# Optimization experiments

Measured on AMD Instinct MI355X. Metric: run time of the kernel, lower is better.

The kernel has to match this reference:

```python
import jax, jax.numpy as jnp
import numpy as np

B, T, D = 2, 2048, 2048
H, DH, DR, DL = 16, 128, 64, 512
WINDOW, STRIDE, GLOBAL = 512, 64, 128
BASE, MAX_SEQ, ORIG_MAX = 10000.0, 131072, 4096
BETA_FAST, BETA_SLOW = 32.0, 1.0
SCALE = 1.0 / np.sqrt(DH)
SCALE_ROPE = 1.0 / np.sqrt(DR)


def _yarn_inv_freq():
    base_inv = 1.0 / (BASE ** (np.arange(0, DR, 2, dtype=np.float32) / DR))
    scale = MAX_SEQ / ORIG_MAX
    freqs = np.arange(DR // 2, dtype=np.float32)
    ramp = np.clip((freqs - BETA_SLOW) / (BETA_FAST - BETA_SLOW), 0.0, 1.0)
    return jnp.asarray(base_inv * (1 - ramp) + (base_inv / scale) * ramp)

_INV_FREQ = _yarn_inv_freq()
_YARN_FACTOR = np.float32(0.1 * np.log(MAX_SEQ / ORIG_MAX) + 1.0)


def _apply_rope(x):
    # x: [B, H, T, DR]
    t = jnp.arange(x.shape[2], dtype=jnp.float32)
    fr = t[:, None] * _INV_FREQ[None, :]            # [T, DR/2]
    emb = jnp.concatenate([fr, fr], axis=-1)        # [T, DR]
    cos, sin = jnp.cos(emb), jnp.sin(emb)
    x1, x2 = jnp.split(x, 2, axis=-1)
    rot = jnp.concatenate([-x2, x1], axis=-1)
    return (x * cos + rot * sin) * _YARN_FACTOR


def _sparse_mask(seq_len):
    pos = jnp.arange(seq_len)
    qp, kp = pos[:, None], pos[None, :]
    dist = qp - kp
    half = WINDOW // 2
    window = (dist >= -half) & (dist <= half)
    dilated = (kp % STRIDE == 0) | (kp < GLOBAL)
    causal = kp <= qp
    return (window | dilated) & causal              # [T, T] bool


def setup_inputs() -> dict:
    key = jax.random.key(0)
    ks = jax.random.split(key, 9)
    s = 0.02
    return {
        "x": jax.random.normal(ks[0], (B, T, D), jnp.float32),
        "w_q": jax.random.normal(ks[1], (D, D), jnp.float32) * s,
        "w_dkv": jax.random.normal(ks[2], (D, DL), jnp.float32) * s,
        "w_uk": jax.random.normal(ks[3], (DL, D), jnp.float32) * s,
        "w_uv": jax.random.normal(ks[4], (DL, D), jnp.float32) * s,
        "w_q_pos": jax.random.normal(ks[5], (D, H * DR), jnp.float32) * s,
        "w_k_pos": jax.random.normal(ks[6], (D, H * DR), jnp.float32) * s,
        "w_o": jax.random.normal(ks[7], (D, D), jnp.float32) * s,
    }


def reference(x, w_q, w_dkv, w_uk, w_uv, w_q_pos, w_k_pos, w_o):
    b, t, _ = x.shape
    # MLA projections
    q_c = (x @ w_q).reshape(b, t, H, DH).transpose(0, 2, 1, 3)      # [B,H,T,DH]
    c_kv = x @ w_dkv                                                # [B,T,DL]
    k_c = (c_kv @ w_uk).reshape(b, t, H, DH).transpose(0, 2, 1, 3)
    v_c = (c_kv @ w_uv).reshape(b, t, H, DH).transpose(0, 2, 1, 3)
    # decoupled RoPE branch (YaRN)
    q_r = (x @ w_q_pos).reshape(b, t, H, DR).transpose(0, 2, 1, 3)
    k_r = (x @ w_k_pos).reshape(b, t, H, DR).transpose(0, 2, 1, 3)
    q_r = _apply_rope(q_r)
    k_r = _apply_rope(k_r)
    # combined content + positional scores
    scores = jnp.einsum("bhqd,bhkd->bhqk", q_c, k_c) * SCALE \
           + jnp.einsum("bhqr,bhkr->bhqk", q_r, k_r) * SCALE_ROPE
    mask = _sparse_mask(t)                                          # [T,T]
    scores = jnp.where(mask[None, None], scores, -jnp.inf)
    attn = jax.nn.softmax(scores, axis=-1)
    out = jnp.einsum("bhqk,bhkd->bhqd", attn, v_c)                  # [B,H,T,DH]
    out = out.transpose(0, 2, 1, 3).reshape(b, t, D)
    return out @ w_o
```

## Files before the change

### kernel.cpp

```cpp
#include <hip/hip_runtime.h>
#include <hip/hip_bf16.h>
#include <cstdint>

typedef __attribute__((ext_vector_type(8))) short short8_t;
typedef __attribute__((ext_vector_type(4))) short short4_t;
typedef __attribute__((ext_vector_type(4))) float f32x4_t;

#define AS1 __attribute__((address_space(1)))
#define AS3 __attribute__((address_space(3)))

__device__ __forceinline__ void gload_lds16(const void* g, void* l) {
  __builtin_amdgcn_global_load_lds((const AS1 void*)g, (AS3 void*)l, 16, 0, 0);
}

__device__ __forceinline__ short8_t ld8(const __hip_bfloat16* p) {
  return *(const short8_t*)p;
}

__global__ __launch_bounds__(256) void k_prep(
    const float* __restrict__ x, __hip_bfloat16* __restrict__ xb,
    const float* __restrict__ wq,  const float* __restrict__ wqp,
    const float* __restrict__ wkp, const float* __restrict__ wdkv,
    const float* __restrict__ wuk, const float* __restrict__ wuv,
    const float* __restrict__ wo,
    __hip_bfloat16* __restrict__ Bt1, __hip_bfloat16* __restrict__ Bt2,
    __hip_bfloat16* __restrict__ woT) {
  __shared__ float t[64][65];
  int bid = blockIdx.x;
  if (bid < 4096) {
    int i = (bid * 256 + threadIdx.x) * 8;
    union { short8_t v; __hip_bfloat16 h[8]; } u;
#pragma unroll
    for (int j = 0; j < 8; ++j) u.h[j] = __float2bfloat16(x[i + j]);
    *(short8_t*)(xb + i) = u.v;
    return;
  }
  bid -= 4096;
  const float* in; __hip_bfloat16* out; int R, C, tile;
  if (bid < 1024)      { in = wq;   out = Bt1;                 R = 2048; C = 2048; tile = bid; }
  else if (bid < 1536) { in = wqp;  out = Bt1 + 2048UL * 2048; R = 2048; C = 1024; tile = bid - 1024; }
  else if (bid < 2048) { in = wkp;  out = Bt1 + 3072UL * 2048; R = 2048; C = 1024; tile = bid - 1536; }
  else if (bid < 2304) { in = wdkv; out = Bt1 + 4096UL * 2048; R = 2048; C = 512;  tile = bid - 2048; }
  else if (bid < 2560) { in = wuk;  out = Bt2;                 R = 512;  C = 2048; tile = bid - 2304; }
  else if (bid < 2816) { in = wuv;  out = Bt2 + 2048UL * 512;  R = 512;  C = 2048; tile = bid - 2560; }
  else                 { in = wo;   out = woT;                 R = 2048; C = 2048; tile = bid - 2816; }
  int nct = C >> 6;
  int ct = tile % nct, rt = tile / nct;
  int r0 = rt << 6, c0 = ct << 6;
#pragma unroll
  for (int i = 0; i < 16; ++i) {
    int idx = i * 256 + threadIdx.x;
    int r = idx >> 6, c = idx & 63;
    t[r][c] = in[(size_t)(r0 + r) * C + c0 + c];
  }
  __syncthreads();
#pragma unroll
  for (int i = 0; i < 16; ++i) {
    int idx = i * 256 + threadIdx.x;
    int c = idx >> 6, r = idx & 63;
    out[(size_t)(c0 + c) * R + r0 + r] = __float2bfloat16(t[r][c]);
  }
}

template<int MODE>
__global__ __launch_bounds__(256) void k_gemm2(const __hip_bfloat16* __restrict__ A,
                                               const __hip_bfloat16* __restrict__ Bt,
                                               int K, int nbx,
                                               void* __restrict__ O0, void* __restrict__ O1,
                                               void* __restrict__ O2, void* __restrict__ O3,
                                               float alpha) {
  __shared__ __align__(16) __hip_bfloat16 Al[3][128 * 32];
  __shared__ __align__(16) __hip_bfloat16 Bl[3][128 * 32];
  int bx = blockIdx.x % nbx, by = blockIdx.x / nbx;
  int tid = threadIdx.x, lane = tid & 63, w = tid >> 6;
  int L = lane & 15, hi = lane >> 4;
  int wr = (w >> 1) << 6, wc = (w & 1) << 6;
  f32x4_t acc[4][4] = {};
  const __hip_bfloat16* Ag = A + (size_t)(by * 128) * K;
  const __hip_bfloat16* Bg = Bt + (size_t)(bx * 128) * K;
  int rA = w * 16 + (lane >> 2);
  int cA = ((lane & 3) ^ ((lane >> 3) & 3)) * 8;
  int NT = K >> 5;

  auto stage = [&](int s) {
    int j = s % 3;
    int k0 = s << 5;
    gload_lds16(Ag + (size_t)rA * K + k0 + cA,        &Al[j][(w * 16) * 32]);
    gload_lds16(Ag + (size_t)(rA + 64) * K + k0 + cA, &Al[j][(64 + w * 16) * 32]);
    gload_lds16(Bg + (size_t)rA * K + k0 + cA,        &Bl[j][(w * 16) * 32]);
    gload_lds16(Bg + (size_t)(rA + 64) * K + k0 + cA, &Bl[j][(64 + w * 16) * 32]);
  };

  stage(0); stage(1);
  asm volatile("s_waitcnt vmcnt(4)\ns_barrier" ::: "memory");

  int hs = hi ^ ((L >> 1) & 3);
  for (int t = 0; t < NT; ++t) {
    int j = t % 3;
    short8_t af[4], bf[4];
#pragma unroll
    for (int m = 0; m < 4; ++m) af[m] = ld8(&Al[j][(wr + 16 * m + L) * 32 + 8 * hs]);
#pragma unroll
    for (int n = 0; n < 4; ++n) bf[n] = ld8(&Bl[j][(wc + 16 * n + L) * 32 + 8 * hs]);
    if (t + 2 < NT) stage(t + 2);
    __builtin_amdgcn_s_setprio(1);
#pragma unroll
    for (int m = 0; m < 4; ++m)
#pragma unroll
      for (int n = 0; n < 4; ++n)
        acc[m][n] = __builtin_amdgcn_mfma_f32_16x16x32_bf16(af[m], bf[n], acc[m][n], 0, 0, 0);
    __builtin_amdgcn_s_setprio(0);
    if (t + 2 < NT)      asm volatile("s_waitcnt vmcnt(4)\ns_barrier" ::: "memory");
    else if (t + 1 < NT) asm volatile("s_waitcnt vmcnt(0)\ns_barrier" ::: "memory");
  }

  int r0 = by * 128 + wr + 4 * hi;
  int cb = bx * 128 + wc;

  if (MODE == 1) {
    float* C = (float*)O0;
    size_t N = (size_t)nbx << 7;
#pragma unroll
    for (int m = 0; m < 4; ++m)
#pragma unroll
      for (int n = 0; n < 4; ++n)
#pragma unroll
        for (int i = 0; i < 4; ++i)
          C[(size_t)(r0 + 16 * m + i) * N + cb + 16 * n + L] = acc[m][n][i] * alpha;
  } else if (MODE == 2) {
    __hip_bfloat16* qcb = (__hip_bfloat16*)O0;
    __hip_bfloat16* qrb = (__hip_bfloat16*)O1;
    __hip_bfloat16* krb = (__hip_bfloat16*)O2;
    __hip_bfloat16* ckv = (__hip_bfloat16*)O3;
    if (bx < 16) {
      const float SCALE = 0.08838834764831845f;
#pragma unroll
      for (int m = 0; m < 4; ++m)
#pragma unroll
        for (int n = 0; n < 4; ++n)
#pragma unroll
          for (int i = 0; i < 4; ++i)
            qcb[(size_t)(r0 + 16 * m + i) * 2048 + cb + 16 * n + L] =
                __float2bfloat16(acc[m][n][i] * SCALE);
    } else if (bx < 32) {
      bool isq = bx < 24;
      __hip_bfloat16* dst = isq ? qrb : krb;
      float osc = isq ? 0.16832169878499666f : 1.3465735902799727f;
      int cbl = cb - (isq ? 2048 : 3072);
      float invf[2];
#pragma unroll
      for (int p = 0; p < 2; ++p) {
        float fi = (float)(16 * p + L);
        float bi = __expf(fi * -0.28782313662425574f);
        float ramp = fminf(fmaxf((fi - 1.0f) * (1.0f / 31.0f), 0.0f), 1.0f);
        invf[p] = bi * (1.0f - ramp * (31.0f / 32.0f));
      }
#pragma unroll
      for (int m = 0; m < 4; ++m)
#pragma unroll
        for (int i = 0; i < 4; ++i) {
          int row = r0 + 16 * m + i;
          float ft = (float)(row & 2047);
#pragma unroll
          for (int p = 0; p < 2; ++p) {
            float sn, cs;
            __sincosf(ft * invf[p], &sn, &cs);
            float x1 = acc[m][p][i], x2 = acc[m][p + 2][i];
            dst[(size_t)row * 1024 + cbl + 16 * p + L] =
                __float2bfloat16((x1 * cs - x2 * sn) * osc);
            dst[(size_t)row * 1024 + cbl + 32 + 16 * p + L] =
                __float2bfloat16((x2 * cs + x1 * sn) * osc);
          }
        }
    } else {
      int cbl = cb - 4096;
#pragma unroll
      for (int m = 0; m < 4; ++m)
#pragma unroll
        for (int n = 0; n < 4; ++n)
#pragma unroll
          for (int i = 0; i < 4; ++i)
            ckv[(size_t)(r0 + 16 * m + i) * 512 + cbl + 16 * n + L] =
                __float2bfloat16(acc[m][n][i]);
    }
  } else if (MODE == 3) {
    __hip_bfloat16* kcb = (__hip_bfloat16*)O0;
    __hip_bfloat16* vcb = (__hip_bfloat16*)O1;
    __hip_bfloat16* vT  = (__hip_bfloat16*)O2;
    if (bx < 16) {
#pragma unroll
      for (int m = 0; m < 4; ++m)
#pragma unroll
        for (int n = 0; n < 4; ++n)
#pragma unroll
          for (int i = 0; i < 4; ++i)
            kcb[(size_t)(r0 + 16 * m + i) * 2048 + cb + 16 * n + L] =
                __float2bfloat16(acc[m][n][i]);
    } else {
#pragma unroll
      for (int m = 0; m < 4; ++m)
#pragma unroll
        for (int n = 0; n < 4; ++n) {
          int vcol = cb - 2048 + 16 * n + L;
          int hh = vcol >> 7, dh = vcol & 127;
          int row0 = r0 + 16 * m;
          int b = row0 >> 11, t0 = row0 & 2047;
          union { short4_t v; __hip_bfloat16 h4[4]; } pk;
#pragma unroll
          for (int i = 0; i < 4; ++i) {
            __hip_bfloat16 bv = __float2bfloat16(acc[m][n][i]);
            vcb[(size_t)(row0 + i) * 2048 + vcol] = bv;
            pk.h4[i] = bv;
          }
          *(short4_t*)(vT + ((size_t)((b * 16 + hh) * 128 + dh) * 2048 + t0)) = pk.v;
        }
    }
  }
}

__global__ __launch_bounds__(256) void k_attn(const __hip_bfloat16* __restrict__ qc,
                                              const __hip_bfloat16* __restrict__ kc,
                                              const __hip_bfloat16* __restrict__ vcb,
                                              const __hip_bfloat16* __restrict__ qr,
                                              const __hip_bfloat16* __restrict__ kr,
                                              const __hip_bfloat16* __restrict__ vT,
                                              __hip_bfloat16* __restrict__ ao) {
  const int T = 2048;
  int bid = blockIdx.x;
  int xcd = bid & 7, r = bid >> 3;
  int j = r >> 5, qt = r & 31;
  int bh = xcd + 8 * j;
  int b = bh >> 4, h = bh & 15;
  int tid = threadIdx.x, lane = tid & 63, w = tid >> 6;
  int L = lane & 15, hi = lane >> 4;
  int q0 = qt * 64;

  __shared__ __align__(16) __hip_bfloat16 Kl[64 * 200];
  __shared__ __align__(16) __hip_bfloat16 Vt[128 * 64];
  __shared__ __align__(16) __hip_bfloat16 Pl[4][16 * 72];

  char* Vtb = (char*)Vt;
  const __hip_bfloat16* vTb = vT + (size_t)(b * 16 + h) * 128 * 2048;

  int qrow = q0 + w * 16 + L;
  size_t qb = (size_t)b * T + qrow;
  short8_t qf[6];
#pragma unroll
  for (int c = 0; c < 4; ++c)
    qf[c] = ld8(qc + qb * 2048 + h * 128 + 32 * c + 8 * hi);
#pragma unroll
  for (int c = 0; c < 2; ++c)
    qf[4 + c] = ld8(qr + qb * 1024 + h * 64 + 32 * c + 8 * hi);

  f32x4_t oacc[8] = {};
  float mrow[4], lrow[4];
#pragma unroll
  for (int i = 0; i < 4; ++i) { mrow[i] = -1e30f; lrow[i] = 0.0f; }

  int nd = qt - 6;

  for (int step = 0; step <= qt + 1; ++step) {
    bool compact = (step == qt + 1);
    if (compact && nd <= 0) break;
    int kt = step;
    if (!compact && kt > 1 && kt < qt - 4) continue;
    int k0 = kt * 64;

    if (!compact) {
#pragma unroll
      for (int i = 0; i < 6; ++i) {
        int ch = i * 256 + tid;
        int rr = ch / 24;
        int d = (ch % 24) * 8;
        size_t krow = (size_t)b * T + k0 + rr;
        const __hip_bfloat16* src = (d < 128)
            ? kc + krow * 2048 + h * 128 + d
            : kr + krow * 1024 + h * 64 + (d - 128);
        *(short8_t*)(Kl + rr * 200 + d) = ld8(src);
      }
#pragma unroll
      for (int i = 0; i < 4; ++i) {
        int ch = i * 256 + tid;
        int row = ch >> 3, c = ch & 7;
        int swc = c ^ (row & 7);
        *(short8_t*)(Vtb + row * 128 + 16 * swc) = ld8(vTb + (size_t)row * 2048 + k0 + c * 8);
      }
    } else {
#pragma unroll
      for (int i = 0; i < 6; ++i) {
        int ch = i * 256 + tid;
        int rr = ch / 24;
        int d = (ch % 24) * 8;
        int srcr = (rr < nd) ? 64 * (2 + rr) : 0;
        size_t krow = (size_t)b * T + srcr;
        const __hip_bfloat16* src = (d < 128)
            ? kc + krow * 2048 + h * 128 + d
            : kr + krow * 1024 + h * 64 + (d - 128);
        *(short8_t*)(Kl + rr * 200 + d) = ld8(src);
      }
#pragma unroll
      for (int i = 0; i < 2; ++i) {
        int ch = i * 256 + tid;
        int jj = ch >> 4, d0 = (ch & 15) * 8;
        if (jj < nd) {
          union { short8_t v; __hip_bfloat16 hh[8]; } u;
          u.v = ld8(vcb + (size_t)(b * 2048 + 64 * (2 + jj)) * 2048 + h * 128 + d0);
#pragma unroll
          for (int qq = 0; qq < 8; ++qq) {
            int dh = d0 + qq;
            int swc = (jj >> 3) ^ (dh & 7);
            *(__hip_bfloat16*)(Vtb + dh * 128 + 16 * swc + 2 * (jj & 7)) = u.hh[qq];
          }
        }
      }
    }
    __syncthreads();

    f32x4_t sacc[4] = {};
    __builtin_amdgcn_s_setprio(1);
#pragma unroll
    for (int n = 0; n < 4; ++n)
#pragma unroll
      for (int c = 0; c < 6; ++c) {
        short8_t bfr = ld8(Kl + (16 * n + L) * 200 + 32 * c + 8 * hi);
        sacc[n] = __builtin_amdgcn_mfma_f32_16x16x32_bf16(qf[c], bfr, sacc[n], 0, 0, 0);
      }
    __builtin_amdgcn_s_setprio(0);

    int rbase = q0 + w * 16 + 4 * hi;
    float p[4][4];
    float mt[4];
#pragma unroll
    for (int i = 0; i < 4; ++i) mt[i] = -1e30f;
#pragma unroll
    for (int n = 0; n < 4; ++n) {
      int col = L + 16 * n;
      int k = k0 + col;
#pragma unroll
      for (int i = 0; i < 4; ++i) {
        int rq = rbase + i;
        bool ok = compact ? (col < nd)
                          : ((k <= rq) && ((rq - k <= 256) || ((k & 63) == 0) || (k < 128)));
        float s = ok ? sacc[n][i] : -1e30f;
        p[n][i] = s;
        mt[i] = fmaxf(mt[i], s);
      }
    }
    for (int d = 1; d < 16; d <<= 1)
#pragma unroll
      for (int i = 0; i < 4; ++i) mt[i] = fmaxf(mt[i], __shfl_xor(mt[i], d, 64));
    float al[4], rs[4];
#pragma unroll
    for (int i = 0; i < 4; ++i) {
      float mnew = fmaxf(mrow[i], mt[i]);
      al[i] = __expf(mrow[i] - mnew);
      mrow[i] = mnew;
      rs[i] = 0.0f;
    }
#pragma unroll
    for (int n = 0; n < 4; ++n)
#pragma unroll
      for (int i = 0; i < 4; ++i) {
        float e = __expf(p[n][i] - mrow[i]);
        p[n][i] = e;
        rs[i] += e;
      }
    for (int d = 1; d < 16; d <<= 1)
#pragma unroll
      for (int i = 0; i < 4; ++i) rs[i] += __shfl_xor(rs[i], d, 64);
#pragma unroll
    for (int i = 0; i < 4; ++i) lrow[i] = lrow[i] * al[i] + rs[i];
#pragma unroll
    for (int n = 0; n < 8; ++n)
#pragma unroll
      for (int i = 0; i < 4; ++i) oacc[n][i] *= al[i];

#pragma unroll
    for (int n = 0; n < 4; ++n)
#pragma unroll
      for (int i = 0; i < 4; ++i)
        Pl[w][(4 * hi + i) * 72 + 16 * n + L] = __float2bfloat16(p[n][i]);
    __syncthreads();

    __builtin_amdgcn_s_setprio(1);
#pragma unroll
    for (int ks = 0; ks < 2; ++ks) {
      short8_t pa = ld8(Pl[w] + L * 72 + 32 * ks + 8 * hi);
#pragma unroll
      for (int n = 0; n < 8; ++n) {
        int vrow = 16 * n + L;
        int chunk = (4 * ks + hi) ^ (vrow & 7);
        short8_t bv = *(const short8_t*)(Vtb + vrow * 128 + 16 * chunk);
        oacc[n] = __builtin_amdgcn_mfma_f32_16x16x32_bf16(pa, bv, oacc[n], 0, 0, 0);
      }
    }
    __builtin_amdgcn_s_setprio(0);
    __syncthreads();
  }

#pragma unroll
  for (int n = 0; n < 8; ++n)
#pragma unroll
    for (int i = 0; i < 4; ++i) {
      int rq = q0 + w * 16 + 4 * hi + i;
      int cdh = 16 * n + L;
      float v = oacc[n][i] / lrow[i];
      ao[((size_t)b * T + rq) * 2048 + h * 128 + cdh] = __float2bfloat16(v);
    }
}

extern "C" void kernel_launch(void* const* d_in, const int* in_sizes, int n_in,
                              void* d_out, int out_size, void* d_ws, size_t ws_size,
                              hipStream_t stream) {
  const float* x     = (const float*)d_in[0];
  const float* w_q   = (const float*)d_in[1];
  const float* w_dkv = (const float*)d_in[2];
  const float* w_uk  = (const float*)d_in[3];
  const float* w_uv  = (const float*)d_in[4];
  const float* w_qp  = (const float*)d_in[5];
  const float* w_kp  = (const float*)d_in[6];
  const float* w_o   = (const float*)d_in[7];
  float* out = (float*)d_out;

  char* ws = (char*)d_ws;
  size_t off = 0;
  auto alloc = [&](size_t elems) {
    __hip_bfloat16* p = (__hip_bfloat16*)(ws + off);
    off += ((elems * 2 + 255) & ~(size_t)255);
    return p;
  };
  __hip_bfloat16* xb  = alloc(8388608);
  __hip_bfloat16* Bt1 = alloc(4608UL * 2048);
  __hip_bfloat16* Bt2 = alloc(4096UL * 512);
  __hip_bfloat16* woT = alloc(4194304);
  __hip_bfloat16* qcb = alloc(8388608);
  __hip_bfloat16* ckv = alloc(2097152);
  __hip_bfloat16* kcb = alloc(8388608);
  __hip_bfloat16* vcb = alloc(8388608);
  __hip_bfloat16* qrb = alloc(4194304);
  __hip_bfloat16* krb = alloc(4194304);
  __hip_bfloat16* aob = alloc(8388608);
  __hip_bfloat16* vT  = alloc(8388608);

  k_prep<<<7936, 256, 0, stream>>>(x, xb, w_q, w_qp, w_kp, w_dkv, w_uk, w_uv, w_o,
                                   Bt1, Bt2, woT);

  k_gemm2<2><<<36 * 32, 256, 0, stream>>>(xb, Bt1, 2048, 36, qcb, qrb, krb, ckv, 1.0f);
  k_gemm2<3><<<32 * 32, 256, 0, stream>>>(ckv, Bt2, 512, 32, kcb, vcb, vT, nullptr, 1.0f);

  k_attn<<<1024, 256, 0, stream>>>(qcb, kcb, vcb, qrb, krb, vT, aob);

  k_gemm2<1><<<16 * 32, 256, 0, stream>>>(aob, woT, 2048, 16, out, nullptr, nullptr, nullptr, 1.0f);
}
```

Before: 268.5 us.

## Read V directly from global in attention, drop vcb buffer, swizzle K/P LDS

Measured after the change: 505.7 us. 1.88x slower.

```diff
diff --git a/kernel.cpp b/kernel.cpp
--- a/kernel.cpp
+++ b/kernel.cpp
@@ -185,8 +185,7 @@
     }
   } else if (MODE == 3) {
     __hip_bfloat16* kcb = (__hip_bfloat16*)O0;
-    __hip_bfloat16* vcb = (__hip_bfloat16*)O1;
-    __hip_bfloat16* vT  = (__hip_bfloat16*)O2;
+    __hip_bfloat16* vT  = (__hip_bfloat16*)O1;
     if (bx < 16) {
 #pragma unroll
       for (int m = 0; m < 4; ++m)
@@ -207,39 +206,34 @@
           int b = row0 >> 11, t0 = row0 & 2047;
           union { short4_t v; __hip_bfloat16 h4[4]; } pk;
 #pragma unroll
-          for (int i = 0; i < 4; ++i) {
-            __hip_bfloat16 bv = __float2bfloat16(acc[m][n][i]);
-            vcb[(size_t)(row0 + i) * 2048 + vcol] = bv;
-            pk.h4[i] = bv;
-          }
+          for (int i = 0; i < 4; ++i) pk.h4[i] = __float2bfloat16(acc[m][n][i]);
           *(short4_t*)(vT + ((size_t)((b * 16 + hh) * 128 + dh) * 2048 + t0)) = pk.v;
         }
     }
   }
 }
 
-__global__ __launch_bounds__(256) void k_attn(const __hip_bfloat16* __restrict__ qc,
-                                              const __hip_bfloat16* __restrict__ kc,
-                                              const __hip_bfloat16* __restrict__ vcb,
-                                              const __hip_bfloat16* __restrict__ qr,
-                                              const __hip_bfloat16* __restrict__ kr,
-                                              const __hip_bfloat16* __restrict__ vT,
-                                              __hip_bfloat16* __restrict__ ao) {
+__global__ __launch_bounds__(256, 4) void k_attn(const __hip_bfloat16* __restrict__ qc,
+                                                 const __hip_bfloat16* __restrict__ kc,
+                                                 const __hip_bfloat16* __restrict__ qr,
+                                                 const __hip_bfloat16* __restrict__ kr,
+                                                 const __hip_bfloat16* __restrict__ vT,
+                                                 __hip_bfloat16* __restrict__ ao) {
   const int T = 2048;
   int bid = blockIdx.x;
   int xcd = bid & 7, r = bid >> 3;
-  int j = r >> 5, qt = r & 31;
-  int bh = xcd + 8 * j;
+  int jg = r >> 5, qt = r & 31;
+  int bh = xcd + 8 * jg;
   int b = bh >> 4, h = bh & 15;
   int tid = threadIdx.x, lane = tid & 63, w = tid >> 6;
   int L = lane & 15, hi = lane >> 4;
   int q0 = qt * 64;
 
-  __shared__ __align__(16) __hip_bfloat16 Kl[64 * 200];
-  __shared__ __align__(16) __hip_bfloat16 Vt[128 * 64];
-  __shared__ __align__(16) __hip_bfloat16 Pl[4][16 * 72];
-
-  char* Vtb = (char*)Vt;
+  __shared__ __align__(16) __hip_bfloat16 Kl[64 * 192];
+  __shared__ __align__(16) __hip_bfloat16 Pl[4][16 * 64];
+  char* Klb = (char*)Kl;
+  char* Plb = (char*)Pl;
+
   const __hip_bfloat16* vTb = vT + (size_t)(b * 16 + h) * 128 * 2048;
 
   int qrow = q0 + w * 16 + L;
@@ -266,65 +260,32 @@
     if (!compact && kt > 1 && kt < qt - 4) continue;
     int k0 = kt * 64;
 
-    if (!compact) {
-#pragma unroll
-      for (int i = 0; i < 6; ++i) {
-        int ch = i * 256 + tid;
-        int rr = ch / 24;
-        int d = (ch % 24) * 8;
-        size_t krow = (size_t)b * T + k0 + rr;
-        const __hip_bfloat16* src = (d < 128)
-            ? kc + krow * 2048 + h * 128 + d
-            : kr + krow * 1024 + h * 64 + (d - 128);
-        *(short8_t*)(Kl + rr * 200 + d) = ld8(src);
-      }
-#pragma unroll
-      for (int i = 0; i < 4; ++i) {
-        int ch = i * 256 + tid;
-        int row = ch >> 3, c = ch & 7;
-        int swc = c ^ (row & 7);
-        *(short8_t*)(Vtb + row * 128 + 16 * swc) = ld8(vTb + (size_t)row * 2048 + k0 + c * 8);
-      }
-    } else {
-#pragma unroll
-      for (int i = 0; i < 6; ++i) {
-        int ch = i * 256 + tid;
-        int rr = ch / 24;
-        int d = (ch % 24) * 8;
-        int srcr = (rr < nd) ? 64 * (2 + rr) : 0;
-        size_t krow = (size_t)b * T + srcr;
-        const __hip_bfloat16* src = (d < 128)
-            ? kc + krow * 2048 + h * 128 + d
-            : kr + krow * 1024 + h * 64 + (d - 128);
-        *(short8_t*)(Kl + rr * 200 + d) = ld8(src);
-      }
-#pragma unroll
-      for (int i = 0; i < 2; ++i) {
-        int ch = i * 256 + tid;
-        int jj = ch >> 4, d0 = (ch & 15) * 8;
-        if (jj < nd) {
-          union { short8_t v; __hip_bfloat16 hh[8]; } u;
-          u.v = ld8(vcb + (size_t)(b * 2048 + 64 * (2 + jj)) * 2048 + h * 128 + d0);
-#pragma unroll
-          for (int qq = 0; qq < 8; ++qq) {
-            int dh = d0 + qq;
-            int swc = (jj >> 3) ^ (dh & 7);
-            *(__hip_bfloat16*)(Vtb + dh * 128 + 16 * swc + 2 * (jj & 7)) = u.hh[qq];
-          }
-        }
-      }
+#pragma unroll
+    for (int i = 0; i < 6; ++i) {
+      int ch = i * 256 + tid;
+      int rr = ch / 24;
+      int c = ch % 24;
+      int d = c * 8;
+      int srcr = compact ? ((rr < nd) ? 64 * (2 + rr) : 0) : (k0 + rr);
+      size_t krow = (size_t)b * T + srcr;
+      const __hip_bfloat16* src = (d < 128)
+          ? kc + krow * 2048 + h * 128 + d
+          : kr + krow * 1024 + h * 64 + (d - 128);
+      *(short8_t*)(Klb + rr * 384 + 16 * (c ^ (rr & 7))) = ld8(src);
     }
     __syncthreads();
 
     f32x4_t sacc[4] = {};
     __builtin_amdgcn_s_setprio(1);
 #pragma unroll
-    for (int n = 0; n < 4; ++n)
+    for (int n = 0; n < 4; ++n) {
+      int row = 16 * n + L;
 #pragma unroll
       for (int c = 0; c < 6; ++c) {
-        short8_t bfr = ld8(Kl + (16 * n + L) * 200 + 32 * c + 8 * hi);
+        short8_t bfr = *(const short8_t*)(Klb + row * 384 + 16 * ((4 * c + hi) ^ (row & 7)));
         sacc[n] = __builtin_amdgcn_mfma_f32_16x16x32_bf16(qf[c], bfr, sacc[n], 0, 0, 0);
       }
+    }
     __builtin_amdgcn_s_setprio(0);
 
     int rbase = q0 + w * 16 + 4 * hi;
@@ -378,20 +339,39 @@
 #pragma unroll
     for (int n = 0; n < 4; ++n)
 #pragma unroll
-      for (int i = 0; i < 4; ++i)
-        Pl[w][(4 * hi + i) * 72 + 16 * n + L] = __float2bfloat16(p[n][i]);
-    __syncthreads();
+      for (int i = 0; i < 4; ++i) {
+        int row = 4 * hi + i;
+        int cc = (2 * n + (L >> 3)) ^ (row & 7);
+        *(__hip_bfloat16*)(Plb + w * 2048 + row * 128 + 16 * cc + 2 * (L & 7)) =
+            __float2bfloat16(p[n][i]);
+      }
 
     __builtin_amdgcn_s_setprio(1);
-#pragma unroll
-    for (int ks = 0; ks < 2; ++ks) {
-      short8_t pa = ld8(Pl[w] + L * 72 + 32 * ks + 8 * hi);
+    if (!compact) {
+#pragma unroll
+      for (int ks = 0; ks < 2; ++ks) {
+        short8_t pa = *(const short8_t*)(Plb + w * 2048 + L * 128 +
+                                         16 * ((4 * ks + hi) ^ (L & 7)));
+#pragma unroll
+        for (int n = 0; n < 8; ++n) {
+          int vrow = 16 * n + L;
+          short8_t bv = ld8(vTb + (size_t)vrow * 2048 + k0 + 32 * ks + 8 * hi);
+          oacc[n] = __builtin_amdgcn_mfma_f32_16x16x32_bf16(pa, bv, oacc[n], 0, 0, 0);
+        }
+      }
+    } else {
+      short8_t pa = *(const short8_t*)(Plb + w * 2048 + L * 128 + 16 * (hi ^ (L & 7)));
 #pragma unroll
       for (int n = 0; n < 8; ++n) {
-        int vrow = 16 * n + L;
-        int chunk = (4 * ks + hi) ^ (vrow & 7);
-        short8_t bv = *(const short8_t*)(Vtb + vrow * 128 + 16 * chunk);
-        oacc[n] = __builtin_amdgcn_mfma_f32_16x16x32_bf16(pa, bv, oacc[n], 0, 0, 0);
+        int dh = 16 * n + L;
+        union { short8_t v; __hip_bfloat16 hh[8]; } u;
+#pragma unroll
+        for (int jj = 0; jj < 8; ++jj) {
+          int jx = 8 * hi + jj;
+          int jc = (jx < nd) ? jx : (nd - 1);
+          u.hh[jj] = vTb[(size_t)dh * 2048 + 64 * (2 + jc)];
+        }
+        oacc[n] = __builtin_amdgcn_mfma_f32_16x16x32_bf16(pa, u.v, oacc[n], 0, 0, 0);
       }
     }
     __builtin_amdgcn_s_setprio(0);
@@ -436,7 +416,6 @@
   __hip_bfloat16* qcb = alloc(8388608);
   __hip_bfloat16* ckv = alloc(2097152);
   __hip_bfloat16* kcb = alloc(8388608);
-  __hip_bfloat16* vcb = alloc(8388608);
   __hip_bfloat16* qrb = alloc(4194304);
   __hip_bfloat16* krb = alloc(4194304);
   __hip_bfloat16* aob = alloc(8388608);
@@ -446,9 +425,9 @@
                                    Bt1, Bt2, woT);
 
   k_gemm2<2><<<36 * 32, 256, 0, stream>>>(xb, Bt1, 2048, 36, qcb, qrb, krb, ckv, 1.0f);
-  k_gemm2<3><<<32 * 32, 256, 0, stream>>>(ckv, Bt2, 512, 32, kcb, vcb, vT, nullptr, 1.0f);
-
-  k_attn<<<1024, 256, 0, stream>>>(qcb, kcb, vcb, qrb, krb, vT, aob);
+  k_gemm2<3><<<32 * 32, 256, 0, stream>>>(ckv, Bt2, 512, 32, kcb, vT, nullptr, nullptr, 1.0f);
+
+  k_attn<<<1024, 256, 0, stream>>>(qcb, kcb, qrb, krb, vT, aob);
 
   k_gemm2<1><<<16 * 32, 256, 0, stream>>>(aob, woT, 2048, 16, out, nullptr, nullptr, nullptr, 1.0f);
 }
```
